# Kernel optimization log

Measured on AMD Instinct MI355X. Metric: run time of the kernel, lower is better.

Reference implementation:

```python
import jax, jax.numpy as jnp
import numpy as np

N = 100000  # nodes
E = 500000  # directed edges (before self-loops)

def _glorot(key, fi, fo):
    s = np.sqrt(6.0 / (fi + fo)).astype(np.float32)
    return jax.random.uniform(key, (fi, fo), jnp.float32, -s, s)

def setup_inputs() -> dict:
    key = jax.random.key(0)
    ks = jax.random.split(key, 6)
    x = jax.random.normal(ks[0], (N, 128), jnp.float32)
    edge_index = jax.random.randint(ks[1], (2, E), 0, N, dtype=jnp.int64)
    return {
        "x": x,
        "edge_index": edge_index,
        "W1": _glorot(ks[2], 128, 512), "b1": jnp.zeros((512,), jnp.float32),
        "W2": _glorot(ks[3], 512, 768), "b2": jnp.zeros((768,), jnp.float32),
        "W3": _glorot(ks[4], 768, 512), "b3": jnp.zeros((512,), jnp.float32),
        "W4": _glorot(ks[5], 512, 128), "b4": jnp.zeros((128,), jnp.float32),
    }

def reference(x, edge_index, W1, b1, W2, b2, W3, b3, W4, b4):
    # PyG GCNConv: add self-loops, deg from dst index, sym-normalized scatter-add.
    loops = jnp.arange(N, dtype=edge_index.dtype)
    src = jnp.concatenate([edge_index[0], loops])  # [E+N]
    dst = jnp.concatenate([edge_index[1], loops])  # [E+N]
    deg = jax.ops.segment_sum(jnp.ones_like(dst, jnp.float32), dst, num_segments=N)
    dinv = jax.lax.rsqrt(deg)  # deg >= 1 thanks to self-loops
    norm = (dinv[src] * dinv[dst])[:, None]  # [E+N, 1]

    def gcn_conv(h, W, b):
        hw = h @ W                                  # [N, Fout] dense linear
        msg = norm * hw[src]                        # [E+N, Fout] gather + scale
        return jax.ops.segment_sum(msg, dst, num_segments=N) + b

    h = jax.nn.gelu(gcn_conv(x, W1, b1), approximate=False)
    h = jax.nn.gelu(gcn_conv(h, W2, b2), approximate=False)
    h = jax.nn.gelu(gcn_conv(h, W3, b3), approximate=False)
    return gcn_conv(h, W4, b4)
```

## Files before the change

kernel.cpp:

```cpp
#include <hip/hip_runtime.h>

typedef short bf16x8 __attribute__((ext_vector_type(8)));
typedef float f32x4 __attribute__((ext_vector_type(4)));

__device__ __forceinline__ float b2f(unsigned short u) {
  union { unsigned int i; float f; } x; x.i = ((unsigned int)u) << 16; return x.f;
}
__device__ __forceinline__ unsigned short f2b(float f) {
  union { float f; unsigned int u; } x; x.f = f;
  unsigned int r = (x.u + 0x7FFFu + ((x.u >> 16) & 1u)) >> 16;
  return (unsigned short)r;
}
__device__ __forceinline__ float gelu_f(float v) {
  return 0.5f * v * (1.0f + erff(v * 0.70710678118654752440f));
}


__global__ void count_kernel(const int* __restrict__ ei, int E, int* __restrict__ cnt) {
  int e = blockIdx.x * 256 + threadIdx.x;
  if (e < E) atomicAdd(&cnt[ei[E + e]], 1);
}

__global__ void dinv_kernel(const int* __restrict__ cnt, float* __restrict__ dinv, int Nn) {
  int n = blockIdx.x * 256 + threadIdx.x;
  if (n < Nn) dinv[n] = rsqrtf((float)cnt[n] + 1.0f);
}

__global__ void xcast_kernel(const float* __restrict__ x, unsigned short* __restrict__ xb,
                             int total8) {
  int i = blockIdx.x * 256 + threadIdx.x;
  if (i < total8) {
    float4 a = *(const float4*)(x + (size_t)i * 8);
    float4 b = *(const float4*)(x + (size_t)i * 8 + 4);
    bf16x8 o;
    o[0] = (short)f2b(a.x); o[1] = (short)f2b(a.y); o[2] = (short)f2b(a.z); o[3] = (short)f2b(a.w);
    o[4] = (short)f2b(b.x); o[5] = (short)f2b(b.y); o[6] = (short)f2b(b.z); o[7] = (short)f2b(b.w);
    *(bf16x8*)(xb + (size_t)i * 8) = o;
  }
}


__global__ __launch_bounds__(256) void scanA_kernel(const int* __restrict__ cnt,
                                                    int* __restrict__ bsum, int Nn) {
  __shared__ int red[256];
  const int t = threadIdx.x;
  const int base = blockIdx.x * 512 + t * 2;
  int a = (base < Nn) ? cnt[base] : 0;
  int b = (base + 1 < Nn) ? cnt[base + 1] : 0;
  red[t] = a + b;
  __syncthreads();
  for (int d = 128; d > 0; d >>= 1) {
    if (t < d) red[t] += red[t + d];
    __syncthreads();
  }
  if (t == 0) bsum[blockIdx.x] = red[0];
}

__global__ __launch_bounds__(256) void scanB_kernel(const int* __restrict__ bsum,
                                                    int* __restrict__ boff,
                                                    int* __restrict__ rowstart,
                                                    int NBLK, int Nn) {
  __shared__ int sh[256];
  const int t = threadIdx.x;
  sh[t] = (t < NBLK) ? bsum[t] : 0;
  __syncthreads();
  for (int d = 1; d < 256; d <<= 1) {
    int x = sh[t];
    int add = (t >= d) ? sh[t - d] : 0;
    __syncthreads();
    sh[t] = x + add;
    __syncthreads();
  }
  if (t < NBLK) boff[t] = (t == 0) ? 0 : sh[t - 1];
  if (t == NBLK - 1) rowstart[Nn] = sh[t];
}

__global__ __launch_bounds__(256) void scanC_kernel(const int* __restrict__ cnt,
                                                    const int* __restrict__ boff,
                                                    int* __restrict__ rowstart,
                                                    int* __restrict__ cursor, int Nn) {
  __shared__ int sh[256];
  const int t = threadIdx.x;
  const int base = blockIdx.x * 512 + t * 2;
  int a = (base < Nn) ? cnt[base] : 0;
  int b = (base + 1 < Nn) ? cnt[base + 1] : 0;
  sh[t] = a + b;
  __syncthreads();
  for (int d = 1; d < 256; d <<= 1) {
    int x = sh[t];
    int add = (t >= d) ? sh[t - d] : 0;
    __syncthreads();
    sh[t] = x + add;
    __syncthreads();
  }
  const int off = boff[blockIdx.x] + ((t == 0) ? 0 : sh[t - 1]);
  if (base < Nn) { rowstart[base] = off; cursor[base] = off; }
  if (base + 1 < Nn) { rowstart[base + 1] = off + a; cursor[base + 1] = off + a; }
}

__global__ void fill_kernel(const int* __restrict__ ei, int E, const float* __restrict__ dinv,
                            int* __restrict__ cursor, int* __restrict__ ssrc,
                            float* __restrict__ snorm) {
  int e = blockIdx.x * 256 + threadIdx.x;
  if (e < E) {
    int s = ei[e], d = ei[E + e];
    int pos = atomicAdd(&cursor[d], 1);
    ssrc[pos] = s;
    snorm[pos] = dinv[s] * dinv[d];
  }
}

__global__ void wtrans_kernel(const float* __restrict__ W, unsigned short* __restrict__ WT,
                              int K, int N) {
  int i = blockIdx.x * 256 + threadIdx.x;
  if (i < K * N) {
    int n = i / K, k = i - n * K;
    WT[i] = f2b(W[k * N + n]);
  }
}


template <int F, bool INF32>
__device__ __forceinline__ void rowload(const void* inv, int row, int base, float* r) {
  constexpr int V = F / 64;
  if constexpr (INF32) {
    const float* in = (const float*)inv + (size_t)row * F + base;
    if constexpr (V == 2) {
      float2 v = *(const float2*)in; r[0] = v.x; r[1] = v.y;
    } else {
      float4 v0 = *(const float4*)in; float4 v1 = *(const float4*)(in + 4);
      r[0] = v0.x; r[1] = v0.y; r[2] = v0.z; r[3] = v0.w;
      r[4] = v1.x; r[5] = v1.y; r[6] = v1.z; r[7] = v1.w;
    }
  } else {
    const unsigned short* in = (const unsigned short*)inv + (size_t)row * F + base;
    if constexpr (V == 2) {
      unsigned int v = *(const unsigned int*)in;
      r[0] = b2f(v & 0xffffu); r[1] = b2f(v >> 16);
    } else {
      bf16x8 v = *(const bf16x8*)in;
#pragma unroll
      for (int i = 0; i < 8; ++i) r[i] = b2f((unsigned short)v[i]);
    }
  }
}

template <int F, int WPN, bool INF32, bool OUTF32, bool HASBIAS, bool DOGELU>
__global__ __launch_bounds__(256) void agg_kernel(
    const int* __restrict__ rowstart, const int* __restrict__ ssrc,
    const float* __restrict__ snorm, const float* __restrict__ dinv,
    const void* __restrict__ inv, const float* __restrict__ bias,
    void* __restrict__ outv, int Nn) {
  constexpr int V = F / 64;
  constexpr int NPB = 4 / WPN;
  const int lane = threadIdx.x & 63;
  const int wid = threadIdx.x >> 6;
  const int nslot = wid / WPN;
  const int sub = wid % WPN;
  const int node = blockIdx.x * NPB + nslot;
  constexpr int CMBSZ = (WPN > 1) ? (NPB * F) : 1;
  __shared__ float cmb[CMBSZ];

  const int base = lane * V;
  float acc[V];
#pragma unroll
  for (int i = 0; i < V; ++i) acc[i] = 0.0f;

  if (node < Nn) {
    if (sub == 0) {
      float w = dinv[node]; w = w * w;
      float rv[V];
      rowload<F, INF32>(inv, node, base, rv);
#pragma unroll
      for (int i = 0; i < V; ++i) acc[i] = w * rv[i];
    }
    const int e0 = rowstart[node], e1 = rowstart[node + 1];
    int e = e0 + sub;
    if constexpr (WPN == 1) {
      for (; e + 4 <= e1; e += 4) {
        int si[4]; float wi[4];
#pragma unroll
        for (int u = 0; u < 4; ++u) { si[u] = ssrc[e + u]; wi[u] = snorm[e + u]; }
        float rv[4][V];
#pragma unroll
        for (int u = 0; u < 4; ++u) rowload<F, INF32>(inv, si[u], base, rv[u]);
#pragma unroll
        for (int u = 0; u < 4; ++u)
#pragma unroll
          for (int i = 0; i < V; ++i) acc[i] += wi[u] * rv[u][i];
      }
      for (; e < e1; ++e) {
        const int s = ssrc[e];
        const float w = snorm[e];
        float rv[V];
        rowload<F, INF32>(inv, s, base, rv);
#pragma unroll
        for (int i = 0; i < V; ++i) acc[i] += w * rv[i];
      }
    } else {
      for (; e + WPN < e1; e += 2 * WPN) {
        int s0 = ssrc[e], s1 = ssrc[e + WPN];
        float w0 = snorm[e], w1 = snorm[e + WPN];
        float r0[V], r1[V];
        rowload<F, INF32>(inv, s0, base, r0);
        rowload<F, INF32>(inv, s1, base, r1);
#pragma unroll
        for (int i = 0; i < V; ++i) acc[i] += w0 * r0[i] + w1 * r1[i];
      }
      if (e < e1) {
        const int s = ssrc[e];
        const float w = snorm[e];
        float rv[V];
        rowload<F, INF32>(inv, s, base, rv);
#pragma unroll
        for (int i = 0; i < V; ++i) acc[i] += w * rv[i];
      }
    }
  }

  if constexpr (WPN > 1) {
    if (sub == 1) {
#pragma unroll
      for (int i = 0; i < V; ++i) cmb[nslot * F + base + i] = acc[i];
    }
    __syncthreads();
    if (sub != 0) return;
#pragma unroll
    for (int i = 0; i < V; ++i) acc[i] += cmb[nslot * F + base + i];
  }
  if (node >= Nn || sub != 0) return;

  if constexpr (HASBIAS) {
#pragma unroll
    for (int i = 0; i < V; ++i) acc[i] += bias[base + i];
  }
  if constexpr (DOGELU) {
#pragma unroll
    for (int i = 0; i < V; ++i) acc[i] = gelu_f(acc[i]);
  }
  if constexpr (OUTF32) {
    float* out = (float*)outv + (size_t)node * F + base;
#pragma unroll
    for (int i = 0; i < V; ++i) out[i] = acc[i];
  } else {
    unsigned short* out = (unsigned short*)outv + (size_t)node * F + base;
    if constexpr (V == 2) {
      unsigned int pack = (unsigned int)f2b(acc[0]) | ((unsigned int)f2b(acc[1]) << 16);
      *(unsigned int*)out = pack;
    } else {
      bf16x8 o;
#pragma unroll
      for (int i = 0; i < 8; ++i) o[i] = (short)f2b(acc[i]);
      *(bf16x8*)out = o;
    }
  }
}


#define GLOAD16(gp, lp)                                                              \
  __builtin_amdgcn_global_load_lds((const __attribute__((address_space(1))) void*)(gp), \
                                   (__attribute__((address_space(3))) void*)(lp), 16, 0, 0)

template <bool HASBIAS, bool DOGELU>
__global__ __launch_bounds__(512, 2) void gemm256(
    const unsigned short* __restrict__ A, const unsigned short* __restrict__ BT,
    const float* __restrict__ bias, unsigned short* __restrict__ C,
    int N, int K, int NT) {
  __shared__ alignas(16) unsigned short smem[65536];
  unsigned short* As = smem;
  unsigned short* Bs = smem + 32768;
  const int tid = threadIdx.x;
  const int lane = tid & 63;
  const int wid = tid >> 6;
  const int wr = wid >> 2;
  const int wc = wid & 3;
  const int rr = lane & 15, rg = lane >> 4;

  const int G = gridDim.x;
  const int q = G >> 3, r = G & 7;
  const int xcd = blockIdx.x & 7, ii = blockIdx.x >> 3;
  const int w = (xcd < r ? xcd * (q + 1) : r * (q + 1) + (xcd - r) * q) + ii;
  const int bx = w / NT;
  const int by = w - bx * NT;
  const size_t brow = (size_t)bx * 256;
  const size_t bcol = (size_t)by * 256;

  const int nt = K >> 6;

  auto stage = [&](int t) {
    const int kb = t << 6;
    const int buf = t & 1;
#pragma unroll
    for (int j = 0; j < 4; ++j) {
      const int s = tid + 512 * j;
      const int row = s >> 3;
      const int lslot = (s & 7) ^ (row & 7);
      GLOAD16(A + (brow + row) * K + kb + lslot * 8, &As[buf * 16384 + s * 8]);
      GLOAD16(BT + (bcol + row) * K + kb + lslot * 8, &Bs[buf * 16384 + s * 8]);
    }
  };

  f32x4 acc[8][4] = {};
  stage(0);
  __syncthreads();
  for (int t = 0; t < nt; ++t) {
    if (t + 1 < nt) stage(t + 1);
    const int buf = t & 1;
    bf16x8 bq[2][4];
#pragma unroll
    for (int kk = 0; kk < 2; ++kk)
#pragma unroll
      for (int nb = 0; nb < 4; ++nb) {
        const int R = wc * 64 + nb * 16 + rr;
        const int ps = (kk * 4 + rg) ^ (R & 7);
        bq[kk][nb] = *(const bf16x8*)(&Bs[buf * 16384 + R * 64 + ps * 8]);
      }
#pragma unroll
    for (int mb = 0; mb < 8; ++mb) {
      const int R = wr * 128 + mb * 16 + rr;
      const int ps0 = rg ^ (R & 7);
      const int ps1 = (4 + rg) ^ (R & 7);
      bf16x8 a0 = *(const bf16x8*)(&As[buf * 16384 + R * 64 + ps0 * 8]);
      bf16x8 a1 = *(const bf16x8*)(&As[buf * 16384 + R * 64 + ps1 * 8]);
#pragma unroll
      for (int nb = 0; nb < 4; ++nb)
        acc[mb][nb] = __builtin_amdgcn_mfma_f32_16x16x32_bf16(a0, bq[0][nb], acc[mb][nb], 0, 0, 0);
#pragma unroll
      for (int nb = 0; nb < 4; ++nb)
        acc[mb][nb] = __builtin_amdgcn_mfma_f32_16x16x32_bf16(a1, bq[1][nb], acc[mb][nb], 0, 0, 0);
    }
    __syncthreads();
  }

  char* Cl = (char*)smem;
#pragma unroll
  for (int mb = 0; mb < 8; ++mb) {
    const int rowl0 = wr * 128 + mb * 16 + rg * 4;
#pragma unroll
    for (int nb = 0; nb < 4; ++nb) {
      const int coll = wc * 64 + nb * 16 + rr;
      float bv = 0.0f;
      if constexpr (HASBIAS) bv = bias[bcol + coll];
#pragma unroll
      for (int r2 = 0; r2 < 4; ++r2) {
        float v = acc[mb][nb][r2] + bv;
        if constexpr (DOGELU) v = gelu_f(v);
        const int rowl = rowl0 + r2;
        *(unsigned short*)(Cl + rowl * 512 + ((coll * 2) ^ ((rowl & 7) << 4))) = f2b(v);
      }
    }
  }
  __syncthreads();
#pragma unroll
  for (int pass = 0; pass < 2; ++pass) {
    const int rowl = pass * 128 + (tid >> 2);
    const int u = tid & 3;
    const size_t gbase = (brow + rowl) * (size_t)N + bcol;
#pragma unroll
    for (int c = 0; c < 8; ++c) {
      uint4 v = *(const uint4*)(Cl + rowl * 512 + ((c * 64 + u * 16) ^ ((rowl & 7) << 4)));
      *(uint4*)(&C[gbase + c * 32 + u * 8]) = v;
    }
  }
}


template <bool HASBIAS, bool DOGELU>
__global__ __launch_bounds__(256) void gemm_bt(
    const unsigned short* __restrict__ A, const unsigned short* __restrict__ BT,
    const float* __restrict__ bias, unsigned short* __restrict__ C,
    int N, int K, int NT) {
  __shared__ alignas(16) unsigned short Asl[128 * 32];
  __shared__ alignas(16) unsigned short Bsl[128 * 32];
  const int tid = threadIdx.x;
  const int lane = tid & 63;
  const int wid = tid >> 6;

  const int G = gridDim.x;
  const int q = G >> 3, r = G & 7;
  const int xcd = blockIdx.x & 7, ii = blockIdx.x >> 3;
  const int w = (xcd < r ? xcd * (q + 1) : r * (q + 1) + (xcd - r) * q) + ii;
  const int bx = w / NT;
  const int by = w - bx * NT;

  const size_t brow = (size_t)bx * 128;
  const size_t bcol = (size_t)by * 128;
  const int wr = (wid >> 1) * 64;
  const int wc = (wid & 1) * 64;
  const int rr = lane & 15, rg = lane >> 4;
  f32x4 acc[4][4] = {};
  const int KT = K >> 5;
  for (int kt = 0; kt < KT; ++kt) {
    const int kb = kt << 5;
#pragma unroll
    for (int rsub = 0; rsub < 2; ++rsub) {
      const int c = tid + rsub * 256;
      const int arow = c >> 2;
      const int jlog = (c & 3) ^ ((arow >> 1) & 3);
      GLOAD16(A + (brow + arow) * K + kb + jlog * 8, &Asl[c * 8]);
      GLOAD16(BT + (bcol + arow) * K + kb + jlog * 8, &Bsl[c * 8]);
    }
    __syncthreads();
    bf16x8 af[4], bfr[4];
#pragma unroll
    for (int m = 0; m < 4; ++m) {
      const int R = wr + m * 16 + rr;
      af[m] = *(const bf16x8*)(&Asl[R * 32 + ((rg ^ ((R >> 1) & 3)) * 8)]);
    }
#pragma unroll
    for (int n = 0; n < 4; ++n) {
      const int R = wc + n * 16 + rr;
      bfr[n] = *(const bf16x8*)(&Bsl[R * 32 + ((rg ^ ((R >> 1) & 3)) * 8)]);
    }
#pragma unroll
    for (int m = 0; m < 4; ++m)
#pragma unroll
      for (int n = 0; n < 4; ++n)
        acc[m][n] = __builtin_amdgcn_mfma_f32_16x16x32_bf16(af[m], bfr[n], acc[m][n], 0, 0, 0);
    __syncthreads();
  }
#pragma unroll
  for (int m = 0; m < 4; ++m) {
    size_t row0 = brow + wr + m * 16 + rg * 4;
#pragma unroll
    for (int n = 0; n < 4; ++n) {
      size_t col = bcol + wc + n * 16 + rr;
      float bv = 0.0f;
      if constexpr (HASBIAS) bv = bias[col];
#pragma unroll
      for (int r2 = 0; r2 < 4; ++r2) {
        float v = acc[m][n][r2] + bv;
        if constexpr (DOGELU) v = gelu_f(v);
        C[(row0 + r2) * N + col] = f2b(v);
      }
    }
  }
}


extern "C" void kernel_launch(void* const* d_in, const int* in_sizes, int n_in,
                              void* d_out, int out_size, void* d_ws, size_t ws_size,
                              hipStream_t stream) {
  const float* x = (const float*)d_in[0];
  const int* ei = (const int*)d_in[1];
  const float* W1 = (const float*)d_in[2]; const float* b1 = (const float*)d_in[3];
  const float* W2 = (const float*)d_in[4]; const float* b2 = (const float*)d_in[5];
  const float* W3 = (const float*)d_in[6]; const float* b3 = (const float*)d_in[7];
  const float* W4 = (const float*)d_in[8]; const float* b4 = (const float*)d_in[9];

  const int Nn = in_sizes[0] / 128;
  const int E = in_sizes[1] / 2;
  const int Mpad = (Nn + 255) & ~255;

  char* p = (char*)d_ws;
  auto alloc = [&](size_t bytes) {
    char* r = p;
    p += (bytes + 255) & ~(size_t)255;
    return r;
  };
  float* dinv = (float*)alloc((size_t)Nn * 4);
  int* cnt = (int*)alloc((size_t)Nn * 4);
  int* rowstart = (int*)alloc((size_t)(Nn + 1) * 4);
  int* cursor = (int*)alloc((size_t)Nn * 4);
  int* ssrc = (int*)alloc((size_t)E * 4);
  float* snorm = (float*)alloc((size_t)E * 4);
  int* bsum = (int*)alloc((size_t)256 * 4);
  int* boff = (int*)alloc((size_t)256 * 4);
  unsigned short* WT1 = (unsigned short*)alloc((size_t)512 * 128 * 2);
  unsigned short* WT2 = (unsigned short*)alloc((size_t)768 * 512 * 2);
  unsigned short* WT3 = (unsigned short*)alloc((size_t)512 * 768 * 2);
  unsigned short* WT4 = (unsigned short*)alloc((size_t)128 * 512 * 2);
  unsigned short* bufA = (unsigned short*)alloc((size_t)Mpad * 512 * 2);
  unsigned short* bufB = (unsigned short*)alloc((size_t)Mpad * 768 * 2);
  unsigned short* xb = bufB;

  const int EB = (E + 255) / 256;
  const int NB = (Nn + 255) / 256;
  const int MT256 = Mpad / 256;
  const int MT128 = Mpad / 128;
  const int NSCAN = (Nn + 511) / 512;

  hipMemsetAsync(cnt, 0, (size_t)Nn * 4, stream);
  count_kernel<<<EB, 256, 0, stream>>>(ei, E, cnt);
  dinv_kernel<<<NB, 256, 0, stream>>>(cnt, dinv, Nn);
  scanA_kernel<<<NSCAN, 256, 0, stream>>>(cnt, bsum, Nn);
  scanB_kernel<<<1, 256, 0, stream>>>(bsum, boff, rowstart, NSCAN, Nn);
  scanC_kernel<<<NSCAN, 256, 0, stream>>>(cnt, boff, rowstart, cursor, Nn);
  fill_kernel<<<EB, 256, 0, stream>>>(ei, E, dinv, cursor, ssrc, snorm);
  wtrans_kernel<<<(128 * 512 + 255) / 256, 256, 0, stream>>>(W1, WT1, 128, 512);
  wtrans_kernel<<<(512 * 768 + 255) / 256, 256, 0, stream>>>(W2, WT2, 512, 768);
  wtrans_kernel<<<(768 * 512 + 255) / 256, 256, 0, stream>>>(W3, WT3, 768, 512);
  wtrans_kernel<<<(512 * 128 + 255) / 256, 256, 0, stream>>>(W4, WT4, 512, 128);
  xcast_kernel<<<(Nn * 16 + 255) / 256, 256, 0, stream>>>(x, xb, Nn * 16);

  agg_kernel<128, 1, false, false, false, false><<<(Nn + 3) / 4, 256, 0, stream>>>(
      rowstart, ssrc, snorm, dinv, xb, nullptr, bufA, Nn);
  gemm256<true, true><<<MT256 * 2, 512, 0, stream>>>(bufA, WT1, b1, bufB, 512, 128, 2);

  agg_kernel<512, 2, false, false, false, false><<<(Nn + 1) / 2, 256, 0, stream>>>(
      rowstart, ssrc, snorm, dinv, bufB, nullptr, bufA, Nn);
  gemm256<true, true><<<MT256 * 3, 512, 0, stream>>>(bufA, WT2, b2, bufB, 768, 512, 3);

  gemm256<false, false><<<MT256 * 2, 512, 0, stream>>>(bufB, WT3, nullptr, bufA, 512, 768, 2);
  agg_kernel<512, 2, false, false, true, true><<<(Nn + 1) / 2, 256, 0, stream>>>(
      rowstart, ssrc, snorm, dinv, bufA, b3, bufB, Nn);

  gemm_bt<false, false><<<MT128 * 1, 256, 0, stream>>>(bufB, WT4, nullptr, bufA, 128, 512, 1);
  agg_kernel<128, 1, false, true, true, false><<<(Nn + 3) / 4, 256, 0, stream>>>(
      rowstart, ssrc, snorm, dinv, bufA, b4, d_out, Nn);
}
```

Measured before the change: 739.9 us.

## Pack CSR edges as int2 records, use one wave per node, swap layer-1 GEMM

Stores each edge's source index and normalization weight together as one int2 record, so the aggregation loop does one 8-byte load per edge instead of two separate loads. The 512-wide aggregation kernels now use one wave per node with 4-way unrolled gathers, replacing the two-wave split with its shared-memory combine and barrier. The first-layer GEMM moves from the 256-tile kernel to the 128-tile gemm_bt kernel. Per-wave work for wide features doubles, which could lower memory-level parallelism on nodes with high degree.

```diff
diff --git a/kernel.cpp b/kernel.cpp
--- a/kernel.cpp
+++ b/kernel.cpp
@@ -99,14 +99,14 @@
 }
 
 __global__ void fill_kernel(const int* __restrict__ ei, int E, const float* __restrict__ dinv,
-                            int* __restrict__ cursor, int* __restrict__ ssrc,
-                            float* __restrict__ snorm) {
+                            int* __restrict__ cursor, int2* __restrict__ erec) {
   int e = blockIdx.x * 256 + threadIdx.x;
   if (e < E) {
     int s = ei[e], d = ei[E + e];
     int pos = atomicAdd(&cursor[d], 1);
-    ssrc[pos] = s;
-    snorm[pos] = dinv[s] * dinv[d];
+    union { float f; int i; } nv;
+    nv.f = dinv[s] * dinv[d];
+    erec[pos] = make_int2(s, nv.i);
   }
 }
 
@@ -145,91 +145,51 @@
   }
 }
 
-template <int F, int WPN, bool INF32, bool OUTF32, bool HASBIAS, bool DOGELU>
+template <int F, bool INF32, bool OUTF32, bool HASBIAS, bool DOGELU>
 __global__ __launch_bounds__(256) void agg_kernel(
-    const int* __restrict__ rowstart, const int* __restrict__ ssrc,
-    const float* __restrict__ snorm, const float* __restrict__ dinv,
+    const int* __restrict__ rowstart, const int2* __restrict__ erec,
+    const float* __restrict__ dinv,
     const void* __restrict__ inv, const float* __restrict__ bias,
     void* __restrict__ outv, int Nn) {
   constexpr int V = F / 64;
-  constexpr int NPB = 4 / WPN;
   const int lane = threadIdx.x & 63;
-  const int wid = threadIdx.x >> 6;
-  const int nslot = wid / WPN;
-  const int sub = wid % WPN;
-  const int node = blockIdx.x * NPB + nslot;
-  constexpr int CMBSZ = (WPN > 1) ? (NPB * F) : 1;
-  __shared__ float cmb[CMBSZ];
-
+  const int node = blockIdx.x * 4 + (threadIdx.x >> 6);
+  if (node >= Nn) return;
   const int base = lane * V;
   float acc[V];
-#pragma unroll
-  for (int i = 0; i < V; ++i) acc[i] = 0.0f;
-
-  if (node < Nn) {
-    if (sub == 0) {
-      float w = dinv[node]; w = w * w;
-      float rv[V];
-      rowload<F, INF32>(inv, node, base, rv);
-#pragma unroll
-      for (int i = 0; i < V; ++i) acc[i] = w * rv[i];
-    }
-    const int e0 = rowstart[node], e1 = rowstart[node + 1];
-    int e = e0 + sub;
-    if constexpr (WPN == 1) {
-      for (; e + 4 <= e1; e += 4) {
-        int si[4]; float wi[4];
-#pragma unroll
-        for (int u = 0; u < 4; ++u) { si[u] = ssrc[e + u]; wi[u] = snorm[e + u]; }
-        float rv[4][V];
-#pragma unroll
-        for (int u = 0; u < 4; ++u) rowload<F, INF32>(inv, si[u], base, rv[u]);
-#pragma unroll
-        for (int u = 0; u < 4; ++u)
-#pragma unroll
-          for (int i = 0; i < V; ++i) acc[i] += wi[u] * rv[u][i];
-      }
-      for (; e < e1; ++e) {
-        const int s = ssrc[e];
-        const float w = snorm[e];
-        float rv[V];
-        rowload<F, INF32>(inv, s, base, rv);
-#pragma unroll
-        for (int i = 0; i < V; ++i) acc[i] += w * rv[i];
-      }
-    } else {
-      for (; e + WPN < e1; e += 2 * WPN) {
-        int s0 = ssrc[e], s1 = ssrc[e + WPN];
-        float w0 = snorm[e], w1 = snorm[e + WPN];
-        float r0[V], r1[V];
-        rowload<F, INF32>(inv, s0, base, r0);
-        rowload<F, INF32>(inv, s1, base, r1);
-#pragma unroll
-        for (int i = 0; i < V; ++i) acc[i] += w0 * r0[i] + w1 * r1[i];
-      }
-      if (e < e1) {
-        const int s = ssrc[e];
-        const float w = snorm[e];
-        float rv[V];
-        rowload<F, INF32>(inv, s, base, rv);
-#pragma unroll
-        for (int i = 0; i < V; ++i) acc[i] += w * rv[i];
-      }
-    }
-  }
-
-  if constexpr (WPN > 1) {
-    if (sub == 1) {
-#pragma unroll
-      for (int i = 0; i < V; ++i) cmb[nslot * F + base + i] = acc[i];
-    }
-    __syncthreads();
-    if (sub != 0) return;
-#pragma unroll
-    for (int i = 0; i < V; ++i) acc[i] += cmb[nslot * F + base + i];
-  }
-  if (node >= Nn || sub != 0) return;
-
+  {
+    float w = dinv[node]; w = w * w;
+    float rv[V];
+    rowload<F, INF32>(inv, node, base, rv);
+#pragma unroll
+    for (int i = 0; i < V; ++i) acc[i] = w * rv[i];
+  }
+  const int e0 = rowstart[node], e1 = rowstart[node + 1];
+  int e = e0;
+  for (; e + 4 <= e1; e += 4) {
+    int si[4]; float wi[4];
+#pragma unroll
+    for (int u = 0; u < 4; ++u) {
+      int2 rec = erec[e + u];
+      si[u] = rec.x;
+      union { int i; float f; } nv; nv.i = rec.y; wi[u] = nv.f;
+    }
+    float rv[4][V];
+#pragma unroll
+    for (int u = 0; u < 4; ++u) rowload<F, INF32>(inv, si[u], base, rv[u]);
+#pragma unroll
+    for (int u = 0; u < 4; ++u)
+#pragma unroll
+      for (int i = 0; i < V; ++i) acc[i] += wi[u] * rv[u][i];
+  }
+  for (; e < e1; ++e) {
+    int2 rec = erec[e];
+    union { int i; float f; } nv; nv.i = rec.y;
+    float rv[V];
+    rowload<F, INF32>(inv, rec.x, base, rv);
+#pragma unroll
+    for (int i = 0; i < V; ++i) acc[i] += nv.f * rv[i];
+  }
   if constexpr (HASBIAS) {
 #pragma unroll
     for (int i = 0; i < V; ++i) acc[i] += bias[base + i];
@@ -462,8 +422,7 @@
   int* cnt = (int*)alloc((size_t)Nn * 4);
   int* rowstart = (int*)alloc((size_t)(Nn + 1) * 4);
   int* cursor = (int*)alloc((size_t)Nn * 4);
-  int* ssrc = (int*)alloc((size_t)E * 4);
-  float* snorm = (float*)alloc((size_t)E * 4);
+  int2* erec = (int2*)alloc((size_t)E * 8);
   int* bsum = (int*)alloc((size_t)256 * 4);
   int* boff = (int*)alloc((size_t)256 * 4);
   unsigned short* WT1 = (unsigned short*)alloc((size_t)512 * 128 * 2);
@@ -476,6 +435,7 @@
 
   const int EB = (E + 255) / 256;
   const int NB = (Nn + 255) / 256;
+  const int AGGB = (Nn + 3) / 4;
   const int MT256 = Mpad / 256;
   const int MT128 = Mpad / 128;
   const int NSCAN = (Nn + 511) / 512;
@@ -486,26 +446,26 @@
   scanA_kernel<<<NSCAN, 256, 0, stream>>>(cnt, bsum, Nn);
   scanB_kernel<<<1, 256, 0, stream>>>(bsum, boff, rowstart, NSCAN, Nn);
   scanC_kernel<<<NSCAN, 256, 0, stream>>>(cnt, boff, rowstart, cursor, Nn);
-  fill_kernel<<<EB, 256, 0, stream>>>(ei, E, dinv, cursor, ssrc, snorm);
+  fill_kernel<<<EB, 256, 0, stream>>>(ei, E, dinv, cursor, erec);
   wtrans_kernel<<<(128 * 512 + 255) / 256, 256, 0, stream>>>(W1, WT1, 128, 512);
   wtrans_kernel<<<(512 * 768 + 255) / 256, 256, 0, stream>>>(W2, WT2, 512, 768);
   wtrans_kernel<<<(768 * 512 + 255) / 256, 256, 0, stream>>>(W3, WT3, 768, 512);
   wtrans_kernel<<<(512 * 128 + 255) / 256, 256, 0, stream>>>(W4, WT4, 512, 128);
   xcast_kernel<<<(Nn * 16 + 255) / 256, 256, 0, stream>>>(x, xb, Nn * 16);
 
-  agg_kernel<128, 1, false, false, false, false><<<(Nn + 3) / 4, 256, 0, stream>>>(
-      rowstart, ssrc, snorm, dinv, xb, nullptr, bufA, Nn);
-  gemm256<true, true><<<MT256 * 2, 512, 0, stream>>>(bufA, WT1, b1, bufB, 512, 128, 2);
-
-  agg_kernel<512, 2, false, false, false, false><<<(Nn + 1) / 2, 256, 0, stream>>>(
-      rowstart, ssrc, snorm, dinv, bufB, nullptr, bufA, Nn);
+  agg_kernel<128, false, false, false, false><<<AGGB, 256, 0, stream>>>(
+      rowstart, erec, dinv, xb, nullptr, bufA, Nn);
+  gemm_bt<true, true><<<MT128 * 4, 256, 0, stream>>>(bufA, WT1, b1, bufB, 512, 128, 4);
+
+  agg_kernel<512, false, false, false, false><<<AGGB, 256, 0, stream>>>(
+      rowstart, erec, dinv, bufB, nullptr, bufA, Nn);
   gemm256<true, true><<<MT256 * 3, 512, 0, stream>>>(bufA, WT2, b2, bufB, 768, 512, 3);
 
   gemm256<false, false><<<MT256 * 2, 512, 0, stream>>>(bufB, WT3, nullptr, bufA, 512, 768, 2);
-  agg_kernel<512, 2, false, false, true, true><<<(Nn + 1) / 2, 256, 0, stream>>>(
-      rowstart, ssrc, snorm, dinv, bufA, b3, bufB, Nn);
+  agg_kernel<512, false, false, true, true><<<AGGB, 256, 0, stream>>>(
+      rowstart, erec, dinv, bufA, b3, bufB, Nn);
 
   gemm_bt<false, false><<<MT128 * 1, 256, 0, stream>>>(bufB, WT4, nullptr, bufA, 128, 512, 1);
-  agg_kernel<128, 1, false, true, true, false><<<(Nn + 3) / 4, 256, 0, stream>>>(
-      rowstart, ssrc, snorm, dinv, bufA, b4, d_out, Nn);
-}
+  agg_kernel<128, false, true, true, false><<<AGGB, 256, 0, stream>>>(
+      rowstart, erec, dinv, bufA, b4, d_out, Nn);
+}
```

Result: faster. 711.0 us (-3.9%).
